# Performance work log

Hardware: AMD Instinct MI355X
Metric: run time of the kernel (lower is better)

The kernel has to match this reference:

```python
import jax, jax.numpy as jnp
import numpy as np

B = 1024
FEATURE_NUM = 13 + 26 * 4000  # 104013 (13 dense + 26 sparse fields, one-hot dim 4000 each)
FIELD_NUM = 13 + 26           # 39
K = 8


def setup_inputs() -> dict:
    key = jax.random.key(0)
    k1, k2, k3 = jax.random.split(key, 3)
    inputs = jax.random.uniform(k1, (B, FEATURE_NUM), dtype=jnp.float32)
    w0 = jnp.zeros((1,), dtype=jnp.float32)
    w = jax.random.normal(k2, (FEATURE_NUM, 1), dtype=jnp.float32) * 0.05
    v = jax.random.normal(k3, (FEATURE_NUM, FIELD_NUM, K), dtype=jnp.float32) * 0.05
    return {"inputs": inputs, "w0": w0, "w": w, "v": v}


def reference(inputs, w0, w, v):
    # linear part: [B, 1]
    linear_part = w0 + inputs @ w
    # field_f: [B, field_num, K] via tensordot over feature axis
    field_f = jnp.tensordot(inputs, v, axes=1)
    # sum over upper triangle (i<j) of <field_f_i, field_f_j> using the
    # sum-square FM identity: 0.5 * (||sum_i f_i||^2 - sum_i ||f_i||^2)
    s = field_f.sum(axis=1)                       # [B, K]
    inter = 0.5 * (jnp.sum(s * s, axis=-1)
                   - jnp.sum(field_f * field_f, axis=(1, 2)))  # [B]
    return linear_part + inter[:, None]           # [B, 1]
```

## Files before the change

### kernel.cpp

```cpp
#include <hip/hip_runtime.h>
#include <stdint.h>

#define B_SZ 1024
#define F_SZ 104013
#define NFIELD 39
#define N_RAW 312
#define N_PAD 320
#define KB_STEPS 3251
#define PART_ELEMS ((size_t)B_SZ * N_PAD)

using bf16x8 = __attribute__((ext_vector_type(8))) short;
using f32x4  = __attribute__((ext_vector_type(4))) float;
typedef float f4u __attribute__((vector_size(16), aligned(4)));

__device__ __forceinline__ unsigned int pack_bf16(float a, float b) {
  unsigned int ua = __float_as_uint(a) + 0x8000u;
  unsigned int ub = __float_as_uint(b) + 0x8000u;
  return (ua >> 16) | (ub & 0xffff0000u);
}

__global__ __launch_bounds__(256) void pack_v(const float* __restrict__ v,
                                              const float* __restrict__ w,
                                              uint4* __restrict__ Bp) {
  const int kb = blockIdx.x;
  const int t  = threadIdx.x;
  __shared__ float vs[32][324];

  for (int idx = t; idx < 32 * 78; idx += 256) {
    int r = idx / 78, c4 = (idx % 78) * 4;
    int k = kb * 32 + r;
    float4 val = make_float4(0.f, 0.f, 0.f, 0.f);
    if (k < F_SZ) val = *(const float4*)(v + (size_t)k * N_RAW + c4);
    *(float4*)&vs[r][c4] = val;
  }
  if (t < 32) {
    int k = kb * 32 + t;
    vs[t][312] = (k < F_SZ) ? w[k] : 0.f;
#pragma unroll
    for (int c = 313; c < 320; ++c) vs[t][c] = 0.f;
  }
  __syncthreads();

#pragma unroll
  for (int i = 0; i < 5; ++i) {
    int p  = t + 256 * i;
    int l  = p & 63;
    int kr = (l >> 4) * 8;
    int col = (p >> 6) * 16 + (l & 15);
    uint4 o;
    o.x = pack_bf16(vs[kr + 0][col], vs[kr + 1][col]);
    o.y = pack_bf16(vs[kr + 2][col], vs[kr + 3][col]);
    o.z = pack_bf16(vs[kr + 4][col], vs[kr + 5][col]);
    o.w = pack_bf16(vs[kr + 6][col], vs[kr + 7][col]);
    Bp[(size_t)kb * 1280 + p] = o;
  }
}

__global__ __launch_bounds__(256, 1) void gemm_split(const float* __restrict__ A,
                                                     const uint4* __restrict__ Bp,
                                                     float* __restrict__ part) {
  const int S  = gridDim.y;
  const int mt = blockIdx.x, s = blockIdx.y;
  const int t  = threadIdx.x;
  const int w  = t >> 6, l = t & 63;
  const int wr = w >> 1, wc = w & 1;
  const int lm = l & 15, lq = l >> 4;
  const int row0 = mt * 128 + wr * 64;
  const int nt0  = wc * 10;
  const int kb0  = (int)((long long)KB_STEPS * s / S);
  const int kb1  = (int)((long long)KB_STEPS * (s + 1) / S);

  f32x4 acc[4][10];
#pragma unroll
  for (int i = 0; i < 4; ++i)
#pragma unroll
    for (int n = 0; n < 10; ++n) acc[i][n] = (f32x4)0.f;

  const float* ap[4];
#pragma unroll
  for (int i = 0; i < 4; ++i)
    ap[i] = A + (size_t)(row0 + i * 16 + lm) * F_SZ + (size_t)kb0 * 32 + lq * 8;
  const uint4* bp = Bp + ((size_t)kb0 * 20 + nt0) * 64 + l;

  for (int kb = kb0; kb < kb1; ++kb) {
    bf16x8 bfrag[10];
#pragma unroll
    for (int n = 0; n < 10; ++n) {
      uint4 bv = bp[n * 64];
      bfrag[n] = __builtin_bit_cast(bf16x8, bv);
    }
    bf16x8 afrag[4];
    if (kb != KB_STEPS - 1) {
#pragma unroll
      for (int i = 0; i < 4; ++i) {
        f4u v0 = *(const f4u*)(ap[i]);
        f4u v1 = *(const f4u*)(ap[i] + 4);
        uint4 pk = make_uint4(pack_bf16(v0[0], v0[1]), pack_bf16(v0[2], v0[3]),
                              pack_bf16(v1[0], v1[1]), pack_bf16(v1[2], v1[3]));
        afrag[i] = __builtin_bit_cast(bf16x8, pk);
      }
    } else {
      int kbase = kb * 32 + lq * 8;
#pragma unroll
      for (int i = 0; i < 4; ++i) {
        float f[8];
#pragma unroll
        for (int j = 0; j < 8; ++j) f[j] = (kbase + j < F_SZ) ? ap[i][j] : 0.f;
        uint4 pk = make_uint4(pack_bf16(f[0], f[1]), pack_bf16(f[2], f[3]),
                              pack_bf16(f[4], f[5]), pack_bf16(f[6], f[7]));
        afrag[i] = __builtin_bit_cast(bf16x8, pk);
      }
    }
#pragma unroll
    for (int i = 0; i < 4; ++i)
#pragma unroll
      for (int n = 0; n < 10; ++n)
        acc[i][n] = __builtin_amdgcn_mfma_f32_16x16x32_bf16(afrag[i], bfrag[n],
                                                            acc[i][n], 0, 0, 0);
#pragma unroll
    for (int i = 0; i < 4; ++i) ap[i] += 32;
    bp += 20 * 64;
  }

  float* out = part + (size_t)s * PART_ELEMS;
#pragma unroll
  for (int i = 0; i < 4; ++i) {
    int rb = row0 + i * 16 + lq * 4;
#pragma unroll
    for (int n = 0; n < 10; ++n) {
      int col = (nt0 + n) * 16 + lm;
#pragma unroll
      for (int r = 0; r < 4; ++r)
        out[(size_t)(rb + r) * N_PAD + col] = acc[i][n][r];
    }
  }
}

__global__ __launch_bounds__(256) void finalize(const float* __restrict__ part,
                                                const float* __restrict__ w0,
                                                float* __restrict__ out, int S) {
  const int b = blockIdx.x;
  const int t = threadIdx.x;
  __shared__ float crow[N_PAD];
  __shared__ float red[4];
  __shared__ float skl[8];

  for (int n = t; n < N_PAD; n += 256) {
    float acc = 0.f;
    for (int s = 0; s < S; ++s)
      acc += part[(size_t)s * PART_ELEMS + (size_t)b * N_PAD + n];
    crow[n] = acc;
  }
  __syncthreads();

  float sq = 0.f;
  for (int n = t; n < N_RAW; n += 256) sq += crow[n] * crow[n];
#pragma unroll
  for (int off = 32; off; off >>= 1) sq += __shfl_down(sq, off);
  if ((t & 63) == 0) red[t >> 6] = sq;
  if (t < 8) {
    float sk = 0.f;
#pragma unroll
    for (int f = 0; f < NFIELD; ++f) sk += crow[f * 8 + t];
    skl[t] = sk;
  }
  __syncthreads();
  if (t == 0) {
    float sumsq = red[0] + red[1] + red[2] + red[3];
    float ss = 0.f;
#pragma unroll
    for (int k = 0; k < 8; ++k) ss += skl[k] * skl[k];
    out[b] = w0[0] + crow[312] + 0.5f * (ss - sumsq);
  }
}

extern "C" void kernel_launch(void* const* d_in, const int* in_sizes, int n_in,
                              void* d_out, int out_size, void* d_ws, size_t ws_size,
                              hipStream_t stream) {
  const float* inputs = (const float*)d_in[0];
  const float* w0 = (const float*)d_in[1];
  const float* w  = (const float*)d_in[2];
  const float* v  = (const float*)d_in[3];
  float* out = (float*)d_out;

  const size_t PART_BYTES   = PART_ELEMS * sizeof(float);
  const size_t PACKED_BYTES = (size_t)KB_STEPS * 20 * 64 * 16;
  int S = 64;
  while (S > 1 && PACKED_BYTES + (size_t)S * PART_BYTES > ws_size) S >>= 1;

  float* part = (float*)d_ws;
  uint4* Bp   = (uint4*)((char*)d_ws + (size_t)S * PART_BYTES);

  pack_v<<<dim3(KB_STEPS), 256, 0, stream>>>(v, w, Bp);
  gemm_split<<<dim3(8, S), 256, 0, stream>>>(inputs, Bp, part);
  finalize<<<dim3(B_SZ), 256, 0, stream>>>(part, w0, out, S);
}
```

Baseline: 784.7 us.

## Stage A and B tiles through double-buffered LDS with direct global-to-LDS loads

The GEMM now uses global_load_lds to copy A rows (fp32) and packed B fragments into a two-slot LDS buffer. The next k-step is prefetched while the current one computes. A is stored with a rotated swizzle to avoid bank conflicts, so the two wave columns share A loads instead of each loading A separately. Launch bounds rise to 2 blocks per CU. The cost is a __syncthreads every k-step and 72 KB of LDS per block, which may limit the 2-block occupancy.

```diff
diff --git a/kernel.cpp b/kernel.cpp
--- a/kernel.cpp
+++ b/kernel.cpp
@@ -11,7 +11,13 @@
 
 using bf16x8 = __attribute__((ext_vector_type(8))) short;
 using f32x4  = __attribute__((ext_vector_type(4))) float;
-typedef float f4u __attribute__((vector_size(16), aligned(4)));
+
+typedef __attribute__((address_space(3))) void* lds_vp;
+typedef const __attribute__((address_space(1))) void* glb_cvp;
+
+__device__ __forceinline__ void ld16(const void* g, void* l) {
+  __builtin_amdgcn_global_load_lds((glb_cvp)g, (lds_vp)l, 16, 0, 0);
+}
 
 __device__ __forceinline__ unsigned int pack_bf16(float a, float b) {
   unsigned int ua = __float_as_uint(a) + 0x8000u;
@@ -56,7 +62,7 @@
   }
 }
 
-__global__ __launch_bounds__(256, 1) void gemm_split(const float* __restrict__ A,
+__global__ __launch_bounds__(256, 2) void gemm_split(const float* __restrict__ A,
                                                      const uint4* __restrict__ Bp,
                                                      float* __restrict__ part) {
   const int S  = gridDim.y;
@@ -65,10 +71,30 @@
   const int w  = t >> 6, l = t & 63;
   const int wr = w >> 1, wc = w & 1;
   const int lm = l & 15, lq = l >> 4;
-  const int row0 = mt * 128 + wr * 64;
-  const int nt0  = wc * 10;
-  const int kb0  = (int)((long long)KB_STEPS * s / S);
-  const int kb1  = (int)((long long)KB_STEPS * (s + 1) / S);
+  const int row0 = mt * 128;
+  const int kb0 = (int)((long long)KB_STEPS * s / S);
+  const int kb1 = (int)((long long)KB_STEPS * (s + 1) / S);
+
+  __shared__ __align__(16) char smem[2][36864];
+
+  const int lr  = l >> 3;
+  const int kgl = ((l & 7) - lr) & 7;
+  size_t arowbase[4];
+#pragma unroll
+  for (int j = 0; j < 4; ++j)
+    arowbase[j] = (size_t)(row0 + (w * 4 + j) * 8 + lr) * F_SZ + (size_t)(kgl * 4);
+
+  auto stage = [&](int kb, int buf, bool withA) {
+    if (withA) {
+#pragma unroll
+      for (int j = 0; j < 4; ++j)
+        ld16(A + arowbase[j] + (size_t)kb * 32, smem[buf] + (w * 4 + j) * 1024);
+    }
+#pragma unroll
+    for (int j = 0; j < 5; ++j)
+      ld16(Bp + ((size_t)kb * 20 + w * 5 + j) * 64 + l,
+           smem[buf] + 16384 + (w * 5 + j) * 1024);
+  };
 
   f32x4 acc[4][10];
 #pragma unroll
@@ -76,59 +102,61 @@
 #pragma unroll
     for (int n = 0; n < 10; ++n) acc[i][n] = (f32x4)0.f;
 
-  const float* ap[4];
-#pragma unroll
-  for (int i = 0; i < 4; ++i)
-    ap[i] = A + (size_t)(row0 + i * 16 + lm) * F_SZ + (size_t)kb0 * 32 + lq * 8;
-  const uint4* bp = Bp + ((size_t)kb0 * 20 + nt0) * 64 + l;
-
+  stage(kb0, 0, true);
+  int cur = 0;
   for (int kb = kb0; kb < kb1; ++kb) {
-    bf16x8 bfrag[10];
-#pragma unroll
-    for (int n = 0; n < 10; ++n) {
-      uint4 bv = bp[n * 64];
-      bfrag[n] = __builtin_bit_cast(bf16x8, bv);
-    }
+    __syncthreads();
+    if (kb + 1 < kb1) stage(kb + 1, cur ^ 1, (kb + 1) != KB_STEPS - 1);
+
     bf16x8 afrag[4];
     if (kb != KB_STEPS - 1) {
+      const char* base = smem[cur];
+      const int rot = lm & 7;
+      const int p0 = (lq * 2 + rot) & 7;
+      const int p1 = (lq * 2 + 1 + rot) & 7;
 #pragma unroll
       for (int i = 0; i < 4; ++i) {
-        f4u v0 = *(const f4u*)(ap[i]);
-        f4u v1 = *(const f4u*)(ap[i] + 4);
-        uint4 pk = make_uint4(pack_bf16(v0[0], v0[1]), pack_bf16(v0[2], v0[3]),
-                              pack_bf16(v1[0], v1[1]), pack_bf16(v1[2], v1[3]));
+        int rowq = wr * 8 + i * 2 + (lm >> 3);
+        f32x4 r0 = *(const f32x4*)(base + rowq * 1024 + rot * 128 + p0 * 16);
+        f32x4 r1 = *(const f32x4*)(base + rowq * 1024 + rot * 128 + p1 * 16);
+        uint4 pk = make_uint4(pack_bf16(r0[0], r0[1]), pack_bf16(r0[2], r0[3]),
+                              pack_bf16(r1[0], r1[1]), pack_bf16(r1[2], r1[3]));
         afrag[i] = __builtin_bit_cast(bf16x8, pk);
       }
     } else {
       int kbase = kb * 32 + lq * 8;
 #pragma unroll
       for (int i = 0; i < 4; ++i) {
+        const float* ap = A + (size_t)(row0 + wr * 64 + i * 16 + lm) * F_SZ;
         float f[8];
 #pragma unroll
-        for (int j = 0; j < 8; ++j) f[j] = (kbase + j < F_SZ) ? ap[i][j] : 0.f;
+        for (int jj = 0; jj < 8; ++jj)
+          f[jj] = (kbase + jj < F_SZ) ? ap[kbase + jj] : 0.f;
         uint4 pk = make_uint4(pack_bf16(f[0], f[1]), pack_bf16(f[2], f[3]),
                               pack_bf16(f[4], f[5]), pack_bf16(f[6], f[7]));
         afrag[i] = __builtin_bit_cast(bf16x8, pk);
       }
     }
-#pragma unroll
-    for (int i = 0; i < 4; ++i)
-#pragma unroll
-      for (int n = 0; n < 10; ++n)
-        acc[i][n] = __builtin_amdgcn_mfma_f32_16x16x32_bf16(afrag[i], bfrag[n],
+
+#pragma unroll
+    for (int n = 0; n < 10; ++n) {
+      bf16x8 bf = __builtin_bit_cast(
+          bf16x8, *(const uint4*)(smem[cur] + 16384 + (wc * 10 + n) * 1024 + l * 16));
+#pragma unroll
+      for (int i = 0; i < 4; ++i)
+        acc[i][n] = __builtin_amdgcn_mfma_f32_16x16x32_bf16(afrag[i], bf,
                                                             acc[i][n], 0, 0, 0);
-#pragma unroll
-    for (int i = 0; i < 4; ++i) ap[i] += 32;
-    bp += 20 * 64;
+    }
+    cur ^= 1;
   }
 
   float* out = part + (size_t)s * PART_ELEMS;
 #pragma unroll
   for (int i = 0; i < 4; ++i) {
-    int rb = row0 + i * 16 + lq * 4;
+    int rb = row0 + wr * 64 + i * 16 + lq * 4;
 #pragma unroll
     for (int n = 0; n < 10; ++n) {
-      int col = (nt0 + n) * 16 + lm;
+      int col = (wc * 10 + n) * 16 + lm;
 #pragma unroll
       for (int r = 0; r < 4; ++r)
         out[(size_t)(rb + r) * N_PAD + col] = acc[i][n][r];
```

Result: faster. 747.7 us (-4.7%).
